# Kernel optimization log

Hardware: AMD Instinct MI355X
Metric: run time of the kernel (lower is better)

Reference implementation:

```python
import jax, jax.numpy as jnp
import numpy as np

B, N, C, H = 4, 1024, 256, 8
HD = C // H
SCALE = HD ** -0.5


def setup_inputs() -> dict:
    key = jax.random.key(0)
    ks = jax.random.split(key, 8)
    x = jax.random.normal(ks[0], (B, N, C), jnp.float32)
    voxel_coord = jax.random.uniform(ks[1], (B, N, 3), jnp.float32)
    # Linear weights stored as [in, out] so y = x @ W + b (same math as torch x @ W.T)
    W_qk = jax.random.normal(ks[2], (C, 2 * C), jnp.float32) * 0.02
    W_v = jax.random.normal(ks[3], (C, C), jnp.float32) * 0.02
    W_proj = jax.random.normal(ks[4], (C, C), jnp.float32) * 0.02
    b_proj = jnp.zeros((C,), jnp.float32)
    W_pos = jax.random.normal(ks[5], (4, H), jnp.float32) * 0.02
    b_pos = jnp.zeros((H,), jnp.float32)
    gating = jnp.ones((H,), jnp.float32)
    return dict(x=x, voxel_coord=voxel_coord, W_qk=W_qk, W_v=W_v,
                W_proj=W_proj, b_proj=b_proj, W_pos=W_pos, b_pos=b_pos,
                gating=gating)


def reference(x, voxel_coord, W_qk, W_v, W_proj, b_proj, W_pos, b_pos, gating):
    b, n, c = x.shape
    # Relative 3D positional encoding: positions[b,i,j] = p[j] - p[i]; feature = [dx,dy,dz,dist]
    diff = voxel_coord[:, None, :, :] - voxel_coord[:, :, None, :]          # [B,N,N,3]
    dist = jnp.sqrt(jnp.sum(diff * diff, axis=-1, keepdims=True))           # [B,N,N,1]
    rel = jnp.concatenate([diff, dist], axis=-1)                            # [B,N,N,4]

    # Positional score per head, softmax over keys j
    pos_logits = jnp.einsum('bijf,fh->bhij', rel, W_pos) + b_pos[None, :, None, None]
    pos_score = jax.nn.softmax(pos_logits, axis=-1)                         # [B,H,N,N]

    # Content score: SDPA with V = I  ==  plain softmax attention matrix
    qk = (x @ W_qk).reshape(b, n, 2, H, HD)
    q = jnp.transpose(qk[:, :, 0], (0, 2, 1, 3))                            # [B,H,N,hd]
    k = jnp.transpose(qk[:, :, 1], (0, 2, 1, 3))
    patch_score = jax.nn.softmax(jnp.einsum('bhid,bhjd->bhij', q, k) * SCALE, axis=-1)

    # Gated mix + renormalize
    sig = jax.nn.sigmoid(gating)[None, :, None, None]
    attn = (1.0 - sig) * patch_score + sig * pos_score
    attn = attn / jnp.sum(attn, axis=-1, keepdims=True)

    v = (x @ W_v).reshape(b, n, H, HD).transpose(0, 2, 1, 3)                # [B,H,N,hd]
    out = jnp.einsum('bhij,bhjd->bihd', attn, v).reshape(b, n, c)           # [B,N,C]
    out = out @ W_proj + b_proj
    return out
```

## Files before the change

kernel.cpp:

```cpp
#include <hip/hip_runtime.h>
#include <hip/hip_bf16.h>

#define LOG2E 1.4426950408889634f

typedef __attribute__((ext_vector_type(8))) short bf16x8_t;
typedef __attribute__((ext_vector_type(4))) float f32x4_t;
typedef __attribute__((ext_vector_type(4))) short s16x4_t;

#if __has_builtin(__builtin_amdgcn_exp2f)
#define EXP2F_(x) __builtin_amdgcn_exp2f(x)
#else
__device__ __forceinline__ float EXP2F_(float x) {
    float r; asm volatile("v_exp_f32 %0, %1\ns_nop 1" : "=v"(r) : "v"(x)); return r;
}
#endif
#if __has_builtin(__builtin_amdgcn_sqrtf)
#define SQRTF_(x) __builtin_amdgcn_sqrtf(x)
#else
__device__ __forceinline__ float SQRTF_(float x) {
    float r; asm volatile("v_sqrt_f32 %0, %1\ns_nop 1" : "=v"(r) : "v"(x)); return r;
}
#endif

__device__ __forceinline__ unsigned short f2bf(float f) {
    unsigned u = __float_as_uint(f);
    u += 0x7fffu + ((u >> 16) & 1u);
    return (unsigned short)(u >> 16);
}

__device__ __forceinline__ unsigned pk2(float lo, float hi) {
    union { __hip_bfloat162 h2; unsigned u; } cvt;
    cvt.h2 = __float22bfloat162_rn(make_float2(lo, hi));
    return cvt.u;
}

__device__ __forceinline__ void stage16(const unsigned short* g, unsigned short* l, int lane) {
#if __has_builtin(__builtin_amdgcn_global_load_lds)
    __builtin_amdgcn_global_load_lds((const __attribute__((address_space(1))) void*)g,
                                     (__attribute__((address_space(3))) void*)l, 16, 0, 0);
#else
    *(uint4*)((char*)l + lane * 16) = *(const uint4*)g;
#endif
}

__device__ __forceinline__ unsigned lds_off(const void* p) {
    return (unsigned)(size_t)(const __attribute__((address_space(3))) void*)p;
}

__device__ __forceinline__ s16x4_t TR16(unsigned addr) {
    s16x4_t r;
    asm volatile("ds_read_b64_tr_b16 %0, %1" : "=v"(r) : "v"(addr) : "memory");
    return r;
}
__device__ __forceinline__ void tr_fence() {
    asm volatile("s_waitcnt lgkmcnt(0)" ::: "memory");
    __builtin_amdgcn_sched_barrier(0);
}

__global__ __launch_bounds__(256) void k_convert(
    const float* __restrict__ Wqk, const float* __restrict__ Wv,
    const float* __restrict__ Wpj, const float* __restrict__ coords,
    const float* __restrict__ W_pos,
    unsigned short* __restrict__ Wqk_t, unsigned short* __restrict__ Wv_t,
    unsigned short* __restrict__ Wp_t, float4* __restrict__ tbl)
{
    __shared__ unsigned short T[64 * 72];
    const int bid = blockIdx.x, tid = threadIdx.x;
    if (bid < 64) {
        const float* src; unsigned short* dst; int N_, kt, nt;
        if (bid < 32)      { src = Wqk; dst = Wqk_t; N_ = 512; kt = bid & 3; nt = bid >> 2; }
        else if (bid < 48) { int t = bid - 32; src = Wv;  dst = Wv_t; N_ = 256; kt = t & 3; nt = t >> 2; }
        else               { int t = bid - 48; src = Wpj; dst = Wp_t; N_ = 256; kt = t & 3; nt = t >> 2; }
        const int kr = tid >> 2, seg = tid & 3;
        #pragma unroll
        for (int u = 0; u < 4; ++u) {
            float4 v = *(const float4*)(src + (kt * 64 + kr) * N_ + nt * 64 + seg * 16 + u * 4);
            T[(seg * 16 + u * 4 + 0) * 72 + kr] = f2bf(v.x);
            T[(seg * 16 + u * 4 + 1) * 72 + kr] = f2bf(v.y);
            T[(seg * 16 + u * 4 + 2) * 72 + kr] = f2bf(v.z);
            T[(seg * 16 + u * 4 + 3) * 72 + kr] = f2bf(v.w);
        }
        __syncthreads();
        const int n = tid >> 2, s2 = tid & 3;
        uint4 a = *(uint4*)&T[n * 72 + s2 * 16];
        uint4 b2 = *(uint4*)&T[n * 72 + s2 * 16 + 8];
        *(uint4*)(dst + (nt * 64 + n) * 256 + kt * 64 + s2 * 16) = a;
        *(uint4*)(dst + (nt * 64 + n) * 256 + kt * 64 + s2 * 16 + 8) = b2;
    } else {
        const int bh = bid - 64, b = bh >> 3, h = bh & 7;
        const float wxl = W_pos[0 * 8 + h] * LOG2E;
        const float wyl = W_pos[1 * 8 + h] * LOG2E;
        const float wzl = W_pos[2 * 8 + h] * LOG2E;
        for (int jl = tid; jl < 1024; jl += 256) {
            float x = coords[(b * 1024 + jl) * 3 + 0];
            float y = coords[(b * 1024 + jl) * 3 + 1];
            float z = coords[(b * 1024 + jl) * 3 + 2];
            tbl[bh * 1024 + jl] = make_float4(x, y, z, fmaf(wxl, x, fmaf(wyl, y, wzl * z)));
        }
    }
}

__global__ __launch_bounds__(256) void k_qkv(
    const float* __restrict__ x,
    const unsigned short* __restrict__ Wqk_t,
    const unsigned short* __restrict__ Wv_t,
    unsigned short* __restrict__ q_ws, unsigned short* __restrict__ k_ws,
    unsigned short* __restrict__ v_ws)
{
    __shared__ unsigned short Al[64 * 64];
    __shared__ unsigned short Bl[64 * 64];
    const int tid = threadIdx.x;
    const int n0 = blockIdx.x * 64;
    const int row0 = blockIdx.y * 64;
    const int w = tid >> 6, lane = tid & 63;
    const int lhi = lane >> 4, llo = lane & 15;
    const unsigned short* Bsrc = (n0 < 512) ? (Wqk_t + n0 * 256) : (Wv_t + (n0 - 512) * 256);

    const int sr = lane >> 3, sc = lane & 7;
    const int scx = sc ^ sr;

    f32x4_t acc[4] = {};
    for (int kc = 0; kc < 4; ++kc) {
        #pragma unroll
        for (int s = 0; s < 2; ++s) {
            int chunk = w * 2 + s;
            int r = chunk * 8 + sr;
            const float* ax = x + (row0 + r) * 256 + kc * 64 + scx * 8;
            float4 a0 = *(const float4*)ax, a1 = *(const float4*)(ax + 4);
            uint4 pk;
            pk.x = pk2(a0.x, a0.y); pk.y = pk2(a0.z, a0.w);
            pk.z = pk2(a1.x, a1.y); pk.w = pk2(a1.z, a1.w);
            *(uint4*)(&Al[r * 64 + sc * 8]) = pk;
            stage16(Bsrc + r * 256 + kc * 64 + scx * 8, &Bl[chunk * 512], lane);
        }
        __syncthreads();
        #pragma unroll
        for (int ks = 0; ks < 2; ++ks) {
            int ua = ((ks * 4 + lhi) ^ (llo & 7)) * 8;
            bf16x8_t a = *(const bf16x8_t*)(&Al[(w * 16 + llo) * 64 + ua]);
            #pragma unroll
            for (int nt = 0; nt < 4; ++nt) {
                bf16x8_t b = *(const bf16x8_t*)(&Bl[(nt * 16 + llo) * 64 + ua]);
                acc[nt] = __builtin_amdgcn_mfma_f32_16x16x32_bf16(a, b, acc[nt], 0, 0, 0);
            }
        }
        __syncthreads();
    }
    constexpr float QSC = (float)(1.4426950408889634 / 5.656854249492380195206754896838);
    #pragma unroll
    for (int nt = 0; nt < 4; ++nt) {
        int ng = n0 + nt * 16 + llo;
        #pragma unroll
        for (int r = 0; r < 4; ++r) {
            int ig = row0 + w * 16 + lhi * 4 + r;
            float val = acc[nt][r];
            int b = ig >> 10, i = ig & 1023;
            if (ng < 256) {
                int h = ng >> 5, d = ng & 31;
                q_ws[((b * 8 + h) * 1024 + i) * 32 + d] = f2bf(val * QSC);
            } else if (ng < 512) {
                int c = ng - 256, h = c >> 5, d = c & 31;
                k_ws[((b * 8 + h) * 1024 + i) * 32 + d] = f2bf(val);
            } else {
                int c = ng - 512, h = c >> 5, d = c & 31;
                v_ws[(size_t)(b * 8 + h) * 32768 +
                     ((i >> 2) * 2 + (d >> 4)) * 64 + (i & 3) * 16 + (d & 15)] = f2bf(val);
            }
        }
    }
}

__global__ __launch_bounds__(512, 2) void k_attn(
    const unsigned short* __restrict__ q_ws,
    const unsigned short* __restrict__ k_ws,
    const unsigned short* __restrict__ v_ws,
    const float4* __restrict__ tbl,
    const float* __restrict__ W_pos,
    const float* __restrict__ b_pos,
    const float* __restrict__ gating,
    unsigned short* __restrict__ o_ws)
{
    __shared__ __align__(16) unsigned short Kl[2 * 64 * 32];
    __shared__ __align__(16) unsigned short Vt[2 * 64 * 32];
    __shared__ __align__(16) unsigned short Wp[2 * 64 * 64];
    __shared__ __align__(16) unsigned short Eq[8 * 64 * 16];

    const int tid = threadIdx.x;
    const int bid = blockIdx.x;
    const int xcd = bid & 7, s = bid >> 3;
    const int bh = xcd * 4 + (s >> 4);
    const int it = s & 15;
    const int b = bh >> 3, h = bh & 7;

    const int w = tid >> 6, lane = tid & 63;
    const int wi = w & 3, wj = w >> 2;
    const int lhi = lane >> 4, llo = lane & 15;

    const float wdl = W_pos[3 * 8 + h] * LOG2E;
    const float bpl = b_pos[h] * LOG2E;

    const int i_base = it * 64 + wi * 16;
    bf16x8_t qf = *(const bf16x8_t*)(q_ws + (bh * 1024 + i_base + llo) * 32 + lhi * 8);

    const float4* tb4 = tbl + (size_t)bh * 1024;
    float xi8[8], yi8[8], zi8[8], ci8[8];
    const bool hsel = (lane & 1);
    #pragma unroll
    for (int e = 0; e < 8; ++e) {
        float4 lo = tb4[i_base + e];
        float4 hi = tb4[i_base + 8 + e];
        xi8[e] = hsel ? hi.x : lo.x;
        yi8[e] = hsel ? hi.y : lo.y;
        zi8[e] = hsel ? hi.z : lo.z;
        ci8[e] = hsel ? hi.w : lo.w;
    }

    bf16x8_t ones;
    #pragma unroll
    for (int e = 0; e < 8; ++e) ones[e] = (short)0x3F80;

    f32x4_t accP[2] = {}, accQ[2] = {};
    f32x4_t accLp = {}, accLq = {};

    const int jl1 = ((lane >> 3) << 2) + ((lane & 7) >> 1);
    unsigned short* eqw = &Eq[w * 1024];
    const unsigned eqbase = lds_off(&Eq[w * 1024]) + lhi * 256 + llo * 8;
    const unsigned vtbase = lds_off(&Vt[wj * 2048]) + lhi * 512 + llo * 8;

    for (int t = 0; t < 8; ++t) {
        const int j0 = wj * 512 + t * 64;
        stage16(k_ws + (bh * 1024 + j0 + wi * 16 + (lane >> 2)) * 32 + (lane & 3) * 8,
                &Kl[wj * 2048 + wi * 512], lane);
        stage16(v_ws + (size_t)bh * 32768 + j0 * 32 + wi * 512 + lane * 8,
                &Vt[wj * 2048 + wi * 512], lane);
        float4 t1 = tb4[j0 + jl1];
        float4 t2 = tb4[j0 + jl1 + 32];
        __syncthreads();

        {
            float aj1 = t1.w + bpl, aj2 = t2.w + bpl;
            float eq1[8], eq2[8];
            #pragma unroll
            for (int e = 0; e < 8; ++e) {
                float dx = t1.x - xi8[e], dy = t1.y - yi8[e], dz = t1.z - zi8[e];
                float d2 = fmaf(dx, dx, fmaf(dy, dy, dz * dz));
                eq1[e] = EXP2F_(fmaf(wdl, SQRTF_(d2), aj1 - ci8[e]));
                float ex = t2.x - xi8[e], ey = t2.y - yi8[e], ez = t2.z - zi8[e];
                float e2 = fmaf(ex, ex, fmaf(ey, ey, ez * ez));
                eq2[e] = EXP2F_(fmaf(wdl, SQRTF_(e2), aj2 - ci8[e]));
            }
            uint4 u1, u2;
            u1.x = pk2(eq1[0], eq1[1]); u1.y = pk2(eq1[2], eq1[3]);
            u1.z = pk2(eq1[4], eq1[5]); u1.w = pk2(eq1[6], eq1[7]);
            u2.x = pk2(eq2[0], eq2[1]); u2.y = pk2(eq2[2], eq2[3]);
            u2.z = pk2(eq2[4], eq2[5]); u2.w = pk2(eq2[6], eq2[7]);
            *(uint4*)(&eqw[lane * 8]) = u1;
            *(uint4*)(&eqw[512 + lane * 8]) = u2;
        }

        #pragma unroll
        for (int jq = 0; jq < 4; ++jq) {
            bf16x8_t kf = *(const bf16x8_t*)(&Kl[wj * 2048 + (jq * 16 + llo) * 32 + lhi * 8]);
            f32x4_t zero = {};
            f32x4_t sv = __builtin_amdgcn_mfma_f32_16x16x32_bf16(kf, qf, zero, 0, 0, 0);
            float ep0 = EXP2F_(sv[0]), ep1 = EXP2F_(sv[1]);
            float ep2 = EXP2F_(sv[2]), ep3 = EXP2F_(sv[3]);
            int off = (wj * 64 + wi * 16 + llo) * 64 +
                      (((jq * 2 + (lhi >> 1)) ^ (llo & 7)) * 8) + (lhi & 1) * 4;
            uint2 uP;
            uP.x = pk2(ep0, ep1); uP.y = pk2(ep2, ep3);
            *(uint2*)(&Wp[off]) = uP;
        }

        #pragma unroll
        for (int jb = 0; jb < 2; ++jb) {
            int uu = ((jb * 4 + lhi) ^ (llo & 7)) * 8;
            bf16x8_t bP = *(const bf16x8_t*)(&Wp[(wj * 64 + wi * 16 + llo) * 64 + uu]);
            s16x4_t q0 = TR16(eqbase + jb * 1024);
            s16x4_t q1 = TR16(eqbase + jb * 1024 + 128);
            s16x4_t a00 = TR16(vtbase + jb * 2048 + 0);
            s16x4_t a01 = TR16(vtbase + jb * 2048 + 256);
            s16x4_t a10 = TR16(vtbase + jb * 2048 + 128);
            s16x4_t a11 = TR16(vtbase + jb * 2048 + 384);
            tr_fence();
            bf16x8_t bQ  = __builtin_shufflevector(q0, q1, 0, 1, 2, 3, 4, 5, 6, 7);
            bf16x8_t af0 = __builtin_shufflevector(a00, a01, 0, 1, 2, 3, 4, 5, 6, 7);
            bf16x8_t af1 = __builtin_shufflevector(a10, a11, 0, 1, 2, 3, 4, 5, 6, 7);
            accLp = __builtin_amdgcn_mfma_f32_16x16x32_bf16(ones, bP, accLp, 0, 0, 0);
            accLq = __builtin_amdgcn_mfma_f32_16x16x32_bf16(ones, bQ, accLq, 0, 0, 0);
            accP[0] = __builtin_amdgcn_mfma_f32_16x16x32_bf16(af0, bP, accP[0], 0, 0, 0);
            accQ[0] = __builtin_amdgcn_mfma_f32_16x16x32_bf16(af0, bQ, accQ[0], 0, 0, 0);
            accP[1] = __builtin_amdgcn_mfma_f32_16x16x32_bf16(af1, bP, accP[1], 0, 0, 0);
            accQ[1] = __builtin_amdgcn_mfma_f32_16x16x32_bf16(af1, bQ, accQ[1], 0, 0, 0);
        }
        __syncthreads();
    }

    float* red = (float*)Wp;
    float* LPQ = (float*)Eq;
    if (wj == 1) {
        float* pr = red + (wi * 64 + lane) * 16;
        *(f32x4_t*)(pr + 0) = accP[0]; *(f32x4_t*)(pr + 4)  = accP[1];
        *(f32x4_t*)(pr + 8) = accQ[0]; *(f32x4_t*)(pr + 12) = accQ[1];
        if (lhi == 0) { LPQ[wi * 16 + llo] = accLp[0]; LPQ[64 + wi * 16 + llo] = accLq[0]; }
    }
    __syncthreads();
    if (wj == 0) {
        const float* pr = red + (wi * 64 + lane) * 16;
        float Lp = accLp[0] + LPQ[wi * 16 + llo];
        float Lq = accLq[0] + LPQ[64 + wi * 16 + llo];
        float sig = 1.0f / (1.0f + __expf(-gating[h]));
        float ca = (1.0f - sig) / Lp, cb2 = sig / Lq;
        int rowg = b * 1024 + it * 64 + wi * 16 + llo;
        #pragma unroll
        for (int dt = 0; dt < 2; ++dt) {
            float o0 = ca * (accP[dt][0] + pr[dt * 4 + 0]) + cb2 * (accQ[dt][0] + pr[8 + dt * 4 + 0]);
            float o1 = ca * (accP[dt][1] + pr[dt * 4 + 1]) + cb2 * (accQ[dt][1] + pr[8 + dt * 4 + 1]);
            float o2 = ca * (accP[dt][2] + pr[dt * 4 + 2]) + cb2 * (accQ[dt][2] + pr[8 + dt * 4 + 2]);
            float o3 = ca * (accP[dt][3] + pr[dt * 4 + 3]) + cb2 * (accQ[dt][3] + pr[8 + dt * 4 + 3]);
            uint2 uu;
            uu.x = pk2(o0, o1); uu.y = pk2(o2, o3);
            *(uint2*)(o_ws + (size_t)rowg * 256 + h * 32 + dt * 16 + lhi * 4) = uu;
        }
    }
}

__global__ __launch_bounds__(256) void k_proj(
    const unsigned short* __restrict__ A,
    const unsigned short* __restrict__ Bt,
    const float* __restrict__ bias,
    float* __restrict__ out)
{
    __shared__ unsigned short Al[64 * 64];
    __shared__ unsigned short Bl[64 * 64];
    const int tid = threadIdx.x;
    const int n0 = blockIdx.x * 64;
    const int row0 = blockIdx.y * 64;
    const int w = tid >> 6, lane = tid & 63;
    const int lhi = lane >> 4, llo = lane & 15;
    const int sr = lane >> 3, sc = lane & 7;
    const int scx = sc ^ sr;

    f32x4_t acc[4] = {};
    for (int kc = 0; kc < 4; ++kc) {
        #pragma unroll
        for (int s = 0; s < 2; ++s) {
            int chunk = w * 2 + s;
            int r = chunk * 8 + sr;
            stage16(A + (row0 + r) * 256 + kc * 64 + scx * 8, &Al[chunk * 512], lane);
            stage16(Bt + (n0 + r) * 256 + kc * 64 + scx * 8, &Bl[chunk * 512], lane);
        }
        __syncthreads();
        #pragma unroll
        for (int ks = 0; ks < 2; ++ks) {
            int ua = ((ks * 4 + lhi) ^ (llo & 7)) * 8;
            bf16x8_t a = *(const bf16x8_t*)(&Al[(w * 16 + llo) * 64 + ua]);
            #pragma unroll
            for (int nt = 0; nt < 4; ++nt) {
                bf16x8_t b = *(const bf16x8_t*)(&Bl[(nt * 16 + llo) * 64 + ua]);
                acc[nt] = __builtin_amdgcn_mfma_f32_16x16x32_bf16(a, b, acc[nt], 0, 0, 0);
            }
        }
        __syncthreads();
    }
    #pragma unroll
    for (int nt = 0; nt < 4; ++nt) {
        int ng = n0 + nt * 16 + llo;
        float bv = bias[ng];
        #pragma unroll
        for (int r = 0; r < 4; ++r) {
            int ig = row0 + w * 16 + lhi * 4 + r;
            out[ig * 256 + ng] = acc[nt][r] + bv;
        }
    }
}

extern "C" void kernel_launch(void* const* d_in, const int* in_sizes, int n_in,
                              void* d_out, int out_size, void* d_ws, size_t ws_size,
                              hipStream_t stream)
{
    const float* x    = (const float*)d_in[0];
    const float* vc   = (const float*)d_in[1];
    const float* Wqk  = (const float*)d_in[2];
    const float* Wv   = (const float*)d_in[3];
    const float* Wpj  = (const float*)d_in[4];
    const float* bpj  = (const float*)d_in[5];
    const float* Wpos = (const float*)d_in[6];
    const float* bpos = (const float*)d_in[7];
    const float* gat  = (const float*)d_in[8];
    float* out = (float*)d_out;

    char* ws = (char*)d_ws;
    unsigned short* Wqk_t = (unsigned short*)(ws + 0);
    unsigned short* Wv_t  = (unsigned short*)(ws + 262144);
    unsigned short* Wp_t  = (unsigned short*)(ws + 393216);
    unsigned short* q_ws  = (unsigned short*)(ws + 524288);
    unsigned short* k_ws  = (unsigned short*)(ws + 2621440);
    unsigned short* v_ws  = (unsigned short*)(ws + 4718592);
    unsigned short* o_ws  = (unsigned short*)(ws + 6815744);
    float4*         tbl   = (float4*)(ws + 8912896);

    hipLaunchKernelGGL(k_convert, dim3(96), dim3(256), 0, stream,
                       Wqk, Wv, Wpj, vc, Wpos, Wqk_t, Wv_t, Wp_t, tbl);
    hipLaunchKernelGGL(k_qkv, dim3(12, 64), dim3(256), 0, stream,
                       x, Wqk_t, Wv_t, q_ws, k_ws, v_ws);
    hipLaunchKernelGGL(k_attn, dim3(512), dim3(512), 0, stream,
                       q_ws, k_ws, v_ws, tbl, Wpos, bpos, gat, o_ws);
    hipLaunchKernelGGL(k_proj, dim3(4, 64), dim3(256), 0, stream,
                       o_ws, Wp_t, bpj, out);
}
```

Measured before the change: 117.5 us.

## Load K/V fragments directly from global and compute positional weights in-register

```diff
diff --git a/kernel.cpp b/kernel.cpp
--- a/kernel.cpp
+++ b/kernel.cpp
@@ -5,7 +5,6 @@
 
 typedef __attribute__((ext_vector_type(8))) short bf16x8_t;
 typedef __attribute__((ext_vector_type(4))) float f32x4_t;
-typedef __attribute__((ext_vector_type(4))) short s16x4_t;
 
 #if __has_builtin(__builtin_amdgcn_exp2f)
 #define EXP2F_(x) __builtin_amdgcn_exp2f(x)
@@ -34,27 +33,13 @@
     return cvt.u;
 }
 
-__device__ __forceinline__ void stage16(const unsigned short* g, unsigned short* l, int lane) {
+__device__ __forceinline__ void stage16(const void* g, void* l, int lane) {
 #if __has_builtin(__builtin_amdgcn_global_load_lds)
     __builtin_amdgcn_global_load_lds((const __attribute__((address_space(1))) void*)g,
                                      (__attribute__((address_space(3))) void*)l, 16, 0, 0);
 #else
     *(uint4*)((char*)l + lane * 16) = *(const uint4*)g;
 #endif
-}
-
-__device__ __forceinline__ unsigned lds_off(const void* p) {
-    return (unsigned)(size_t)(const __attribute__((address_space(3))) void*)p;
-}
-
-__device__ __forceinline__ s16x4_t TR16(unsigned addr) {
-    s16x4_t r;
-    asm volatile("ds_read_b64_tr_b16 %0, %1" : "=v"(r) : "v"(addr) : "memory");
-    return r;
-}
-__device__ __forceinline__ void tr_fence() {
-    asm volatile("s_waitcnt lgkmcnt(0)" ::: "memory");
-    __builtin_amdgcn_sched_barrier(0);
 }
 
 __global__ __launch_bounds__(256) void k_convert(
@@ -150,27 +135,33 @@
     #pragma unroll
     for (int nt = 0; nt < 4; ++nt) {
         int ng = n0 + nt * 16 + llo;
-        #pragma unroll
-        for (int r = 0; r < 4; ++r) {
-            int ig = row0 + w * 16 + lhi * 4 + r;
-            float val = acc[nt][r];
-            int b = ig >> 10, i = ig & 1023;
-            if (ng < 256) {
-                int h = ng >> 5, d = ng & 31;
-                q_ws[((b * 8 + h) * 1024 + i) * 32 + d] = f2bf(val * QSC);
-            } else if (ng < 512) {
-                int c = ng - 256, h = c >> 5, d = c & 31;
-                k_ws[((b * 8 + h) * 1024 + i) * 32 + d] = f2bf(val);
-            } else {
-                int c = ng - 512, h = c >> 5, d = c & 31;
-                v_ws[(size_t)(b * 8 + h) * 32768 +
-                     ((i >> 2) * 2 + (d >> 4)) * 64 + (i & 3) * 16 + (d & 15)] = f2bf(val);
+        if (ng < 512) {
+            #pragma unroll
+            for (int r = 0; r < 4; ++r) {
+                int ig = row0 + w * 16 + lhi * 4 + r;
+                float val = acc[nt][r];
+                int b = ig >> 10, i = ig & 1023;
+                if (ng < 256) {
+                    int h = ng >> 5, d = ng & 31;
+                    q_ws[((b * 8 + h) * 1024 + i) * 32 + d] = f2bf(val * QSC);
+                } else {
+                    int c = ng - 256, h = c >> 5, d = c & 31;
+                    k_ws[((b * 8 + h) * 1024 + i) * 32 + d] = f2bf(val);
+                }
             }
-        }
-    }
-}
-
-__global__ __launch_bounds__(512, 2) void k_attn(
+        } else {
+            int c = ng - 512, h = c >> 5, d = c & 31;
+            int i0 = row0 + w * 16 + lhi * 4;
+            int b = i0 >> 10, i = i0 & 1023;
+            uint2 vv;
+            vv.x = pk2(acc[nt][0], acc[nt][1]);
+            vv.y = pk2(acc[nt][2], acc[nt][3]);
+            *(uint2*)(v_ws + (size_t)(b * 8 + h) * 32768 + ((i >> 3) * 32 + d) * 8 + (i & 7)) = vv;
+        }
+    }
+}
+
+__global__ __launch_bounds__(512, 4) void k_attn(
     const unsigned short* __restrict__ q_ws,
     const unsigned short* __restrict__ k_ws,
     const unsigned short* __restrict__ v_ws,
@@ -180,10 +171,8 @@
     const float* __restrict__ gating,
     unsigned short* __restrict__ o_ws)
 {
-    __shared__ __align__(16) unsigned short Kl[2 * 64 * 32];
-    __shared__ __align__(16) unsigned short Vt[2 * 64 * 32];
-    __shared__ __align__(16) unsigned short Wp[2 * 64 * 64];
-    __shared__ __align__(16) unsigned short Eq[8 * 64 * 16];
+    __shared__ __align__(16) float4 TBL[1024];
+    __shared__ __align__(16) unsigned short Wp[8 * 16 * 64];
 
     const int tid = threadIdx.x;
     const int bid = blockIdx.x;
@@ -203,16 +192,14 @@
     bf16x8_t qf = *(const bf16x8_t*)(q_ws + (bh * 1024 + i_base + llo) * 32 + lhi * 8);
 
     const float4* tb4 = tbl + (size_t)bh * 1024;
-    float xi8[8], yi8[8], zi8[8], ci8[8];
-    const bool hsel = (lane & 1);
+    float4 icst = tb4[i_base + llo];
+    const float xi = icst.x, yi = icst.y, zi = icst.z;
+    const float cmb = bpl - icst.w;
+
     #pragma unroll
-    for (int e = 0; e < 8; ++e) {
-        float4 lo = tb4[i_base + e];
-        float4 hi = tb4[i_base + 8 + e];
-        xi8[e] = hsel ? hi.x : lo.x;
-        yi8[e] = hsel ? hi.y : lo.y;
-        zi8[e] = hsel ? hi.z : lo.z;
-        ci8[e] = hsel ? hi.w : lo.w;
+    for (int r = 0; r < 2; ++r) {
+        int sidx = w * 128 + r * 64 + lane;
+        stage16(tb4 + (sidx ^ ((sidx >> 3) & 7)), &TBL[w * 128 + r * 64], lane);
     }
 
     bf16x8_t ones;
@@ -222,82 +209,71 @@
     f32x4_t accP[2] = {}, accQ[2] = {};
     f32x4_t accLp = {}, accLq = {};
 
-    const int jl1 = ((lane >> 3) << 2) + ((lane & 7) >> 1);
-    unsigned short* eqw = &Eq[w * 1024];
-    const unsigned eqbase = lds_off(&Eq[w * 1024]) + lhi * 256 + llo * 8;
-    const unsigned vtbase = lds_off(&Vt[wj * 2048]) + lhi * 512 + llo * 8;
+    const unsigned short* kbase = k_ws + (size_t)bh * 32768;
+    const unsigned short* vbase = v_ws + (size_t)bh * 32768;
+
+    __syncthreads();
 
     for (int t = 0; t < 8; ++t) {
         const int j0 = wj * 512 + t * 64;
-        stage16(k_ws + (bh * 1024 + j0 + wi * 16 + (lane >> 2)) * 32 + (lane & 3) * 8,
-                &Kl[wj * 2048 + wi * 512], lane);
-        stage16(v_ws + (size_t)bh * 32768 + j0 * 32 + wi * 512 + lane * 8,
-                &Vt[wj * 2048 + wi * 512], lane);
-        float4 t1 = tb4[j0 + jl1];
-        float4 t2 = tb4[j0 + jl1 + 32];
-        __syncthreads();
-
-        {
-            float aj1 = t1.w + bpl, aj2 = t2.w + bpl;
-            float eq1[8], eq2[8];
+        bf16x8_t kf[4], vf[4];
+        #pragma unroll
+        for (int jq = 0; jq < 4; ++jq)
+            kf[jq] = *(const bf16x8_t*)(kbase + (j0 + jq * 16 + llo) * 32 + lhi * 8);
+        #pragma unroll
+        for (int jb = 0; jb < 2; ++jb)
+            #pragma unroll
+            for (int dt = 0; dt < 2; ++dt)
+                vf[jb * 2 + dt] = *(const bf16x8_t*)(vbase +
+                    ((j0 + jb * 32 + lhi * 8) >> 3) * 256 + (dt * 16 + llo) * 8);
+
+        bf16x8_t bQ[2];
+        #pragma unroll
+        for (int jb = 0; jb < 2; ++jb) {
+            int jj = j0 + jb * 32 + lhi * 8;
+            int xs = (jj >> 3) & 7;
+            float eq[8];
             #pragma unroll
             for (int e = 0; e < 8; ++e) {
-                float dx = t1.x - xi8[e], dy = t1.y - yi8[e], dz = t1.z - zi8[e];
+                float4 cj = TBL[jj + (e ^ xs)];
+                float dx = cj.x - xi, dy = cj.y - yi, dz = cj.z - zi;
                 float d2 = fmaf(dx, dx, fmaf(dy, dy, dz * dz));
-                eq1[e] = EXP2F_(fmaf(wdl, SQRTF_(d2), aj1 - ci8[e]));
-                float ex = t2.x - xi8[e], ey = t2.y - yi8[e], ez = t2.z - zi8[e];
-                float e2 = fmaf(ex, ex, fmaf(ey, ey, ez * ez));
-                eq2[e] = EXP2F_(fmaf(wdl, SQRTF_(e2), aj2 - ci8[e]));
+                eq[e] = EXP2F_(fmaf(wdl, SQRTF_(d2), cj.w + cmb));
             }
-            uint4 u1, u2;
-            u1.x = pk2(eq1[0], eq1[1]); u1.y = pk2(eq1[2], eq1[3]);
-            u1.z = pk2(eq1[4], eq1[5]); u1.w = pk2(eq1[6], eq1[7]);
-            u2.x = pk2(eq2[0], eq2[1]); u2.y = pk2(eq2[2], eq2[3]);
-            u2.z = pk2(eq2[4], eq2[5]); u2.w = pk2(eq2[6], eq2[7]);
-            *(uint4*)(&eqw[lane * 8]) = u1;
-            *(uint4*)(&eqw[512 + lane * 8]) = u2;
+            uint4 uq;
+            uq.x = pk2(eq[0], eq[1]); uq.y = pk2(eq[2], eq[3]);
+            uq.z = pk2(eq[4], eq[5]); uq.w = pk2(eq[6], eq[7]);
+            bQ[jb] = *(bf16x8_t*)&uq;
         }
 
         #pragma unroll
         for (int jq = 0; jq < 4; ++jq) {
-            bf16x8_t kf = *(const bf16x8_t*)(&Kl[wj * 2048 + (jq * 16 + llo) * 32 + lhi * 8]);
             f32x4_t zero = {};
-            f32x4_t sv = __builtin_amdgcn_mfma_f32_16x16x32_bf16(kf, qf, zero, 0, 0, 0);
-            float ep0 = EXP2F_(sv[0]), ep1 = EXP2F_(sv[1]);
-            float ep2 = EXP2F_(sv[2]), ep3 = EXP2F_(sv[3]);
-            int off = (wj * 64 + wi * 16 + llo) * 64 +
+            f32x4_t sv = __builtin_amdgcn_mfma_f32_16x16x32_bf16(kf[jq], qf, zero, 0, 0, 0);
+            uint2 uP;
+            uP.x = pk2(EXP2F_(sv[0]), EXP2F_(sv[1]));
+            uP.y = pk2(EXP2F_(sv[2]), EXP2F_(sv[3]));
+            int off = (w * 16 + llo) * 64 +
                       (((jq * 2 + (lhi >> 1)) ^ (llo & 7)) * 8) + (lhi & 1) * 4;
-            uint2 uP;
-            uP.x = pk2(ep0, ep1); uP.y = pk2(ep2, ep3);
             *(uint2*)(&Wp[off]) = uP;
         }
 
         #pragma unroll
         for (int jb = 0; jb < 2; ++jb) {
-            int uu = ((jb * 4 + lhi) ^ (llo & 7)) * 8;
-            bf16x8_t bP = *(const bf16x8_t*)(&Wp[(wj * 64 + wi * 16 + llo) * 64 + uu]);
-            s16x4_t q0 = TR16(eqbase + jb * 1024);
-            s16x4_t q1 = TR16(eqbase + jb * 1024 + 128);
-            s16x4_t a00 = TR16(vtbase + jb * 2048 + 0);
-            s16x4_t a01 = TR16(vtbase + jb * 2048 + 256);
-            s16x4_t a10 = TR16(vtbase + jb * 2048 + 128);
-            s16x4_t a11 = TR16(vtbase + jb * 2048 + 384);
-            tr_fence();
-            bf16x8_t bQ  = __builtin_shufflevector(q0, q1, 0, 1, 2, 3, 4, 5, 6, 7);
-            bf16x8_t af0 = __builtin_shufflevector(a00, a01, 0, 1, 2, 3, 4, 5, 6, 7);
-            bf16x8_t af1 = __builtin_shufflevector(a10, a11, 0, 1, 2, 3, 4, 5, 6, 7);
+            bf16x8_t bP = *(const bf16x8_t*)(&Wp[(w * 16 + llo) * 64 +
+                                                 (((jb * 4 + lhi) ^ (llo & 7)) * 8)]);
             accLp = __builtin_amdgcn_mfma_f32_16x16x32_bf16(ones, bP, accLp, 0, 0, 0);
-            accLq = __builtin_amdgcn_mfma_f32_16x16x32_bf16(ones, bQ, accLq, 0, 0, 0);
-            accP[0] = __builtin_amdgcn_mfma_f32_16x16x32_bf16(af0, bP, accP[0], 0, 0, 0);
-            accQ[0] = __builtin_amdgcn_mfma_f32_16x16x32_bf16(af0, bQ, accQ[0], 0, 0, 0);
-            accP[1] = __builtin_amdgcn_mfma_f32_16x16x32_bf16(af1, bP, accP[1], 0, 0, 0);
-            accQ[1] = __builtin_amdgcn_mfma_f32_16x16x32_bf16(af1, bQ, accQ[1], 0, 0, 0);
-        }
-        __syncthreads();
-    }
-
+            accLq = __builtin_amdgcn_mfma_f32_16x16x32_bf16(ones, bQ[jb], accLq, 0, 0, 0);
+            accP[0] = __builtin_amdgcn_mfma_f32_16x16x32_bf16(vf[jb * 2 + 0], bP, accP[0], 0, 0, 0);
+            accP[1] = __builtin_amdgcn_mfma_f32_16x16x32_bf16(vf[jb * 2 + 1], bP, accP[1], 0, 0, 0);
+            accQ[0] = __builtin_amdgcn_mfma_f32_16x16x32_bf16(vf[jb * 2 + 0], bQ[jb], accQ[0], 0, 0, 0);
+            accQ[1] = __builtin_amdgcn_mfma_f32_16x16x32_bf16(vf[jb * 2 + 1], bQ[jb], accQ[1], 0, 0, 0);
+        }
+    }
+
+    __syncthreads();
     float* red = (float*)Wp;
-    float* LPQ = (float*)Eq;
+    float* LPQ = (float*)TBL;
     if (wj == 1) {
         float* pr = red + (wi * 64 + lane) * 16;
         *(f32x4_t*)(pr + 0) = accP[0]; *(f32x4_t*)(pr + 4)  = accP[1];
```

After: 115.4 us. About the same (-1.8%).
